# Optimization experiments

Measured on AMD Instinct MI355X. Metric: run time of the kernel, lower is better.

Reference implementation:

```python
import jax, jax.numpy as jnp
import numpy as np

B, OBS, NH, LAT = 8192, 256, 2048, 128

def setup_inputs() -> dict:
    key = jax.random.key(0)
    k1, k2, k3, k4, k5, k6 = jax.random.split(key, 6)
    s1 = 1.0 / np.sqrt(OBS + NH)
    s2 = 1.0 / np.sqrt(NH)
    return {
        "x": jax.random.normal(k1, (B, OBS), dtype=jnp.float32),
        "h": jax.random.normal(k2, (B, NH), dtype=jnp.float32),
        "W_i2h": jax.random.normal(k3, (NH, OBS + NH), dtype=jnp.float32) * s1,
        "b_i2h": jax.random.normal(k4, (NH,), dtype=jnp.float32) * s1,
        "W_h2o": jax.random.normal(k5, (2 * LAT, NH), dtype=jnp.float32) * s2,
        "b_h2o": jax.random.normal(k6, (2 * LAT,), dtype=jnp.float32) * s2,
    }

def reference(x, h, W_i2h, b_i2h, W_h2o, b_h2o):
    # combined = cat((x, h), dim=1)  -> [B, OBS+NH]
    combined = jnp.concatenate([x, h], axis=1)
    # h_new = tanh(i2h(combined));  Linear is y = x @ W.T + b
    h_new = jnp.tanh(combined @ W_i2h.T + b_i2h)
    out = h_new @ W_h2o.T + b_h2o  # [B, 2*LAT]
    return (out, h_new)
```

## Files before the change

### kernel.cpp

```cpp
#include <hip/hip_runtime.h>
#include <hip/hip_bf16.h>
#include <cstdint>

using bf16 = __hip_bfloat16;
typedef __attribute__((ext_vector_type(8))) short short8;
typedef __attribute__((ext_vector_type(4))) float floatx4;

static constexpr int BATCH = 8192;
static constexpr int K1    = 2304;
static constexpr int N1    = 2048;
static constexpr int K2    = 2048;
static constexpr int N2    = 256;

__device__ __forceinline__ void gload_lds16(const void* g, void* l) {
  __builtin_amdgcn_global_load_lds(
      (const __attribute__((address_space(1))) void*)g,
      (__attribute__((address_space(3))) void*)l, 16, 0, 0);
}

__device__ __forceinline__ float fast_tanh(float x) {
  float e = __builtin_amdgcn_exp2f(x * 2.8853900817779268f);
  return 1.0f - 2.0f * __builtin_amdgcn_rcpf(e + 1.0f);
}

__global__ __launch_bounds__(256) void cvt_f32_to_bf16(
    const float* __restrict__ s, bf16* __restrict__ d, int n8) {
  int i = blockIdx.x * 256 + threadIdx.x;
  if (i >= n8) return;
  const float4* sp = (const float4*)s + (size_t)i * 2;
  float4 a = sp[0], b = sp[1];
  union { short8 v; bf16 e[8]; } u;
  u.e[0] = __float2bfloat16(a.x); u.e[1] = __float2bfloat16(a.y);
  u.e[2] = __float2bfloat16(a.z); u.e[3] = __float2bfloat16(a.w);
  u.e[4] = __float2bfloat16(b.x); u.e[5] = __float2bfloat16(b.y);
  u.e[6] = __float2bfloat16(b.z); u.e[7] = __float2bfloat16(b.w);
  *(short8*)(d + (size_t)i * 8) = u.v;
}

__global__ __launch_bounds__(256) void build_combined(
    const float* __restrict__ x, const float* __restrict__ h,
    bf16* __restrict__ comb) {
  int i = blockIdx.x * 256 + threadIdx.x;
  int row  = i / 288;
  int slot = i - row * 288;
  const float* src = (slot < 32) ? (x + (size_t)row * 256 + slot * 8)
                                 : (h + (size_t)row * 2048 + (slot - 32) * 8);
  float4 a = ((const float4*)src)[0];
  float4 b = ((const float4*)src)[1];
  union { short8 v; bf16 e[8]; } u;
  u.e[0] = __float2bfloat16(a.x); u.e[1] = __float2bfloat16(a.y);
  u.e[2] = __float2bfloat16(a.z); u.e[3] = __float2bfloat16(a.w);
  u.e[4] = __float2bfloat16(b.x); u.e[5] = __float2bfloat16(b.y);
  u.e[6] = __float2bfloat16(b.z); u.e[7] = __float2bfloat16(b.w);
  *(short8*)(comb + (size_t)row * 2304 + slot * 8) = u.v;
}

__global__ __launch_bounds__(256) void bias_init(
    const float* __restrict__ bias, float* __restrict__ out) {
  int i = blockIdx.x * 256 + threadIdx.x;
  float4 b = ((const float4*)bias)[i & 63];
  ((float4*)out)[i] = b;
}

__global__ __launch_bounds__(256) void gemm1_tanh(
    const bf16* __restrict__ A, const bf16* __restrict__ W,
    const float* __restrict__ bias,
    float* __restrict__ hf32, bf16* __restrict__ hb16) {
  __shared__ bf16 As[128 * 64];
  __shared__ bf16 Bs[128 * 64];
  const int t    = threadIdx.x;
  const int lane = t & 63;
  const int wave = t >> 6;
  const int wm   = (wave & 1) * 64;
  const int wn   = (wave >> 1) * 64;
  const int quad = lane >> 4;
  const int r15  = lane & 15;
  const int srow = t >> 3;
  const int sc   = t & 7;

  const size_t Abase = (size_t)blockIdx.x * 128 * K1;
  const size_t Bbase = (size_t)blockIdx.y * 128 * K1;

  floatx4 acc[4][4];
  const floatx4 z = {0.f, 0.f, 0.f, 0.f};
#pragma unroll
  for (int i = 0; i < 4; i++)
#pragma unroll
    for (int j = 0; j < 4; j++) acc[i][j] = z;

  for (int kt = 0; kt < K1 / 64; ++kt) {
    const int k0 = kt * 64;
    __syncthreads();
#pragma unroll
    for (int it = 0; it < 4; ++it) {
      int row = it * 32 + srow;
      int gc  = k0 + ((sc ^ (row & 7)) << 3);
      gload_lds16(A + Abase + (size_t)row * K1 + gc,
                  (char*)As + it * 4096 + t * 16);
    }
#pragma unroll
    for (int it = 0; it < 4; ++it) {
      int row = it * 32 + srow;
      int gc  = k0 + ((sc ^ (row & 7)) << 3);
      gload_lds16(W + Bbase + (size_t)row * K1 + gc,
                  (char*)Bs + it * 4096 + t * 16);
    }
    __syncthreads();
#pragma unroll
    for (int ks = 0; ks < 2; ++ks) {
      short8 af[4], bfr[4];
      const int kq = ks * 4 + quad;
#pragma unroll
      for (int mt = 0; mt < 4; ++mt) {
        int row = wm + mt * 16 + r15;
        af[mt] = *(const short8*)((const char*)As + row * 128 +
                                  ((kq ^ (row & 7)) << 4));
      }
#pragma unroll
      for (int nt = 0; nt < 4; ++nt) {
        int row = wn + nt * 16 + r15;
        bfr[nt] = *(const short8*)((const char*)Bs + row * 128 +
                                   ((kq ^ (row & 7)) << 4));
      }
#pragma unroll
      for (int mt = 0; mt < 4; ++mt)
#pragma unroll
        for (int nt = 0; nt < 4; ++nt)
          acc[mt][nt] = __builtin_amdgcn_mfma_f32_16x16x32_bf16(
              af[mt], bfr[nt], acc[mt][nt], 0, 0, 0);
    }
  }

  const int gcol0 = blockIdx.y * 128 + wn;
  float bv[4];
#pragma unroll
  for (int nt = 0; nt < 4; ++nt) bv[nt] = bias[gcol0 + nt * 16 + r15];
  const size_t grow0 = (size_t)blockIdx.x * 128 + wm;
#pragma unroll
  for (int mt = 0; mt < 4; ++mt) {
#pragma unroll
    for (int i = 0; i < 4; ++i) {
      size_t gr = grow0 + mt * 16 + quad * 4 + i;
      size_t rb = gr * (size_t)N1;
#pragma unroll
      for (int nt = 0; nt < 4; ++nt) {
        int gc = gcol0 + nt * 16 + r15;
        float v = fast_tanh(acc[mt][nt][i] + bv[nt]);
        hf32[rb + gc] = v;
        hb16[rb + gc] = __float2bfloat16(v);
      }
    }
  }
}

__global__ __launch_bounds__(256) void gemm2_splitk(
    const bf16* __restrict__ A, const bf16* __restrict__ W,
    float* __restrict__ out) {
  __shared__ bf16 As[128 * 64];
  __shared__ bf16 Bs[64 * 64];
  const int t    = threadIdx.x;
  const int lane = t & 63;
  const int wave = t >> 6;
  const int wm   = (wave & 1) * 64;
  const int wn   = (wave >> 1) * 32;
  const int quad = lane >> 4;
  const int r15  = lane & 15;
  const int srow = t >> 3;
  const int sc   = t & 7;

  const size_t Abase = (size_t)blockIdx.x * 128 * K2;
  const size_t Bbase = (size_t)blockIdx.y * 64 * K2;
  const int ks0 = blockIdx.z * (K2 / 4);

  floatx4 acc[4][2];
  const floatx4 z = {0.f, 0.f, 0.f, 0.f};
#pragma unroll
  for (int i = 0; i < 4; i++) { acc[i][0] = z; acc[i][1] = z; }

  for (int kt = 0; kt < 8; ++kt) {
    const int k0 = ks0 + kt * 64;
    __syncthreads();
#pragma unroll
    for (int it = 0; it < 4; ++it) {
      int row = it * 32 + srow;
      int gc  = k0 + ((sc ^ (row & 7)) << 3);
      gload_lds16(A + Abase + (size_t)row * K2 + gc,
                  (char*)As + it * 4096 + t * 16);
    }
#pragma unroll
    for (int it = 0; it < 2; ++it) {
      int row = it * 32 + srow;
      int gc  = k0 + ((sc ^ (row & 7)) << 3);
      gload_lds16(W + Bbase + (size_t)row * K2 + gc,
                  (char*)Bs + it * 4096 + t * 16);
    }
    __syncthreads();
#pragma unroll
    for (int ks = 0; ks < 2; ++ks) {
      short8 af[4], bfr[2];
      const int kq = ks * 4 + quad;
#pragma unroll
      for (int mt = 0; mt < 4; ++mt) {
        int row = wm + mt * 16 + r15;
        af[mt] = *(const short8*)((const char*)As + row * 128 +
                                  ((kq ^ (row & 7)) << 4));
      }
#pragma unroll
      for (int nt = 0; nt < 2; ++nt) {
        int row = wn + nt * 16 + r15;
        bfr[nt] = *(const short8*)((const char*)Bs + row * 128 +
                                   ((kq ^ (row & 7)) << 4));
      }
#pragma unroll
      for (int mt = 0; mt < 4; ++mt)
#pragma unroll
        for (int nt = 0; nt < 2; ++nt)
          acc[mt][nt] = __builtin_amdgcn_mfma_f32_16x16x32_bf16(
              af[mt], bfr[nt], acc[mt][nt], 0, 0, 0);
    }
  }

  const int gcol0 = blockIdx.y * 64 + wn;
  const size_t grow0 = (size_t)blockIdx.x * 128 + wm;
#pragma unroll
  for (int mt = 0; mt < 4; ++mt) {
#pragma unroll
    for (int i = 0; i < 4; ++i) {
      size_t gr = grow0 + mt * 16 + quad * 4 + i;
      size_t rb = gr * (size_t)N2;
#pragma unroll
      for (int nt = 0; nt < 2; ++nt) {
        int gc = gcol0 + nt * 16 + r15;
        unsafeAtomicAdd(&out[rb + gc], acc[mt][nt][i]);
      }
    }
  }
}

extern "C" void kernel_launch(void* const* d_in, const int* in_sizes, int n_in,
                              void* d_out, int out_size, void* d_ws,
                              size_t ws_size, hipStream_t stream) {
  const float* x     = (const float*)d_in[0];
  const float* h     = (const float*)d_in[1];
  const float* W_i2h = (const float*)d_in[2];
  const float* b_i2h = (const float*)d_in[3];
  const float* W_h2o = (const float*)d_in[4];
  const float* b_h2o = (const float*)d_in[5];

  float* out       = (float*)d_out;
  float* hnew_f32  = out + (size_t)BATCH * N2;

  bf16* comb   = (bf16*)d_ws;
  bf16* Wi2h_b = comb + (size_t)BATCH * K1;
  bf16* Wh2o_b = Wi2h_b + (size_t)N1 * K1;
  bf16* hnew_b = Wh2o_b + (size_t)N2 * K2;

  bias_init<<<(BATCH * N2 / 4) / 256, 256, 0, stream>>>(b_h2o, out);

  build_combined<<<(BATCH * (K1 / 8)) / 256, 256, 0, stream>>>(x, h, comb);
  cvt_f32_to_bf16<<<((N1 * K1 / 8) + 255) / 256, 256, 0, stream>>>(
      W_i2h, Wi2h_b, N1 * K1 / 8);
  cvt_f32_to_bf16<<<((N2 * K2 / 8) + 255) / 256, 256, 0, stream>>>(
      W_h2o, Wh2o_b, N2 * K2 / 8);

  gemm1_tanh<<<dim3(BATCH / 128, N1 / 128), 256, 0, stream>>>(
      comb, Wi2h_b, b_i2h, hnew_f32, hnew_b);

  gemm2_splitk<<<dim3(BATCH / 128, N2 / 64, 4), 256, 0, stream>>>(
      hnew_b, Wh2o_b, out);
}
```

Measured before the change: 297.3 us.

## Merge conversion kernels into one prep launch and retile second GEMM

The three fp32-to-bf16 conversion kernels become one launch that picks its segment from the thread index, removing two kernel launches and their gaps. The second GEMM is retiled so each block covers 32 rows and all 256 output columns, with split-K reduced from 4 to 2. Each block now reads its A rows once instead of once per column tile, and there are half as many atomic adds per output. The cost is loading the full 256-row W tile into LDS every k-step, and the new 256x2 grid has less parallelism per block.

```diff
diff --git a/kernel.cpp b/kernel.cpp
--- a/kernel.cpp
+++ b/kernel.cpp
@@ -23,28 +23,7 @@
   return 1.0f - 2.0f * __builtin_amdgcn_rcpf(e + 1.0f);
 }
 
-__global__ __launch_bounds__(256) void cvt_f32_to_bf16(
-    const float* __restrict__ s, bf16* __restrict__ d, int n8) {
-  int i = blockIdx.x * 256 + threadIdx.x;
-  if (i >= n8) return;
-  const float4* sp = (const float4*)s + (size_t)i * 2;
-  float4 a = sp[0], b = sp[1];
-  union { short8 v; bf16 e[8]; } u;
-  u.e[0] = __float2bfloat16(a.x); u.e[1] = __float2bfloat16(a.y);
-  u.e[2] = __float2bfloat16(a.z); u.e[3] = __float2bfloat16(a.w);
-  u.e[4] = __float2bfloat16(b.x); u.e[5] = __float2bfloat16(b.y);
-  u.e[6] = __float2bfloat16(b.z); u.e[7] = __float2bfloat16(b.w);
-  *(short8*)(d + (size_t)i * 8) = u.v;
-}
-
-__global__ __launch_bounds__(256) void build_combined(
-    const float* __restrict__ x, const float* __restrict__ h,
-    bf16* __restrict__ comb) {
-  int i = blockIdx.x * 256 + threadIdx.x;
-  int row  = i / 288;
-  int slot = i - row * 288;
-  const float* src = (slot < 32) ? (x + (size_t)row * 256 + slot * 8)
-                                 : (h + (size_t)row * 2048 + (slot - 32) * 8);
+__device__ __forceinline__ short8 cvt8(const float* src) {
   float4 a = ((const float4*)src)[0];
   float4 b = ((const float4*)src)[1];
   union { short8 v; bf16 e[8]; } u;
@@ -52,7 +31,30 @@
   u.e[2] = __float2bfloat16(a.z); u.e[3] = __float2bfloat16(a.w);
   u.e[4] = __float2bfloat16(b.x); u.e[5] = __float2bfloat16(b.y);
   u.e[6] = __float2bfloat16(b.z); u.e[7] = __float2bfloat16(b.w);
-  *(short8*)(comb + (size_t)row * 2304 + slot * 8) = u.v;
+  return u.v;
+}
+
+static constexpr int SEG0 = BATCH * (K1 / 8);
+static constexpr int SEG1 = N1 * K1 / 8;
+static constexpr int SEG2 = N2 * K2 / 8;
+__global__ __launch_bounds__(256) void prep(
+    const float* __restrict__ x, const float* __restrict__ h,
+    const float* __restrict__ W1, const float* __restrict__ W2,
+    bf16* __restrict__ comb, bf16* __restrict__ W1b, bf16* __restrict__ W2b) {
+  int i = blockIdx.x * 256 + threadIdx.x;
+  if (i < SEG0) {
+    int row  = i / 288;
+    int slot = i - row * 288;
+    const float* src = (slot < 32) ? (x + (size_t)row * 256 + slot * 8)
+                                   : (h + (size_t)row * 2048 + (slot - 32) * 8);
+    *(short8*)(comb + (size_t)row * 2304 + slot * 8) = cvt8(src);
+  } else if (i < SEG0 + SEG1) {
+    int j = i - SEG0;
+    *(short8*)(W1b + (size_t)j * 8) = cvt8(W1 + (size_t)j * 8);
+  } else {
+    int j = i - (SEG0 + SEG1);
+    *(short8*)(W2b + (size_t)j * 8) = cvt8(W2 + (size_t)j * 8);
+  }
 }
 
 __global__ __launch_bounds__(256) void bias_init(
@@ -153,83 +155,79 @@
   }
 }
 
-__global__ __launch_bounds__(256) void gemm2_splitk(
+__global__ __launch_bounds__(256) void gemm2_out(
     const bf16* __restrict__ A, const bf16* __restrict__ W,
     float* __restrict__ out) {
-  __shared__ bf16 As[128 * 64];
-  __shared__ bf16 Bs[64 * 64];
+  __shared__ bf16 As[32 * 64];
+  __shared__ bf16 Bs[256 * 64];
   const int t    = threadIdx.x;
   const int lane = t & 63;
   const int wave = t >> 6;
-  const int wm   = (wave & 1) * 64;
-  const int wn   = (wave >> 1) * 32;
   const int quad = lane >> 4;
   const int r15  = lane & 15;
   const int srow = t >> 3;
   const int sc   = t & 7;
 
-  const size_t Abase = (size_t)blockIdx.x * 128 * K2;
-  const size_t Bbase = (size_t)blockIdx.y * 64 * K2;
-  const int ks0 = blockIdx.z * (K2 / 4);
-
-  floatx4 acc[4][2];
+  const int mrow0 = blockIdx.x * 32;
+  const int kbase = blockIdx.y * (K2 / 2);
+
+  floatx4 acc[2][4];
   const floatx4 z = {0.f, 0.f, 0.f, 0.f};
 #pragma unroll
-  for (int i = 0; i < 4; i++) { acc[i][0] = z; acc[i][1] = z; }
-
-  for (int kt = 0; kt < 8; ++kt) {
-    const int k0 = ks0 + kt * 64;
-    __syncthreads();
-#pragma unroll
-    for (int it = 0; it < 4; ++it) {
+  for (int i = 0; i < 2; i++)
+#pragma unroll
+    for (int j = 0; j < 4; j++) acc[i][j] = z;
+
+  for (int kt = 0; kt < 16; ++kt) {
+    const int k0 = kbase + kt * 64;
+    __syncthreads();
+    {
+      int row = srow;
+      int gc  = k0 + ((sc ^ (row & 7)) << 3);
+      gload_lds16(A + (size_t)(mrow0 + row) * K2 + gc, (char*)As + t * 16);
+    }
+#pragma unroll
+    for (int it = 0; it < 8; ++it) {
       int row = it * 32 + srow;
       int gc  = k0 + ((sc ^ (row & 7)) << 3);
-      gload_lds16(A + Abase + (size_t)row * K2 + gc,
-                  (char*)As + it * 4096 + t * 16);
-    }
-#pragma unroll
-    for (int it = 0; it < 2; ++it) {
-      int row = it * 32 + srow;
-      int gc  = k0 + ((sc ^ (row & 7)) << 3);
-      gload_lds16(W + Bbase + (size_t)row * K2 + gc,
+      gload_lds16(W + (size_t)row * K2 + gc,
                   (char*)Bs + it * 4096 + t * 16);
     }
     __syncthreads();
 #pragma unroll
     for (int ks = 0; ks < 2; ++ks) {
-      short8 af[4], bfr[2];
+      short8 af[2], bfr[4];
       const int kq = ks * 4 + quad;
 #pragma unroll
-      for (int mt = 0; mt < 4; ++mt) {
-        int row = wm + mt * 16 + r15;
+      for (int mt = 0; mt < 2; ++mt) {
+        int row = mt * 16 + r15;
         af[mt] = *(const short8*)((const char*)As + row * 128 +
                                   ((kq ^ (row & 7)) << 4));
       }
 #pragma unroll
-      for (int nt = 0; nt < 2; ++nt) {
-        int row = wn + nt * 16 + r15;
+      for (int nt = 0; nt < 4; ++nt) {
+        int row = wave * 64 + nt * 16 + r15;
         bfr[nt] = *(const short8*)((const char*)Bs + row * 128 +
                                    ((kq ^ (row & 7)) << 4));
       }
 #pragma unroll
-      for (int mt = 0; mt < 4; ++mt)
-#pragma unroll
-        for (int nt = 0; nt < 2; ++nt)
+      for (int mt = 0; mt < 2; ++mt)
+#pragma unroll
+        for (int nt = 0; nt < 4; ++nt)
           acc[mt][nt] = __builtin_amdgcn_mfma_f32_16x16x32_bf16(
               af[mt], bfr[nt], acc[mt][nt], 0, 0, 0);
     }
   }
 
-  const int gcol0 = blockIdx.y * 64 + wn;
-  const size_t grow0 = (size_t)blockIdx.x * 128 + wm;
-#pragma unroll
-  for (int mt = 0; mt < 4; ++mt) {
+  const int gcol0 = wave * 64;
+#pragma unroll
+  for (int mt = 0; mt < 2; ++mt) {
 #pragma unroll
     for (int i = 0; i < 4; ++i) {
-      size_t gr = grow0 + mt * 16 + quad * 4 + i;
+      size_t gr = (size_t)mrow0 + mt * 16 + quad * 4 + i;
       size_t rb = gr * (size_t)N2;
 #pragma unroll
-      for (int nt = 0; nt < 2; ++nt) {
+      for (int nt = 0; nt < 4; ++nt) {
         int gc = gcol0 + nt * 16 + r15;
         unsafeAtomicAdd(&out[rb + gc], acc[mt][nt][i]);
       }
@@ -257,15 +255,11 @@
 
   bias_init<<<(BATCH * N2 / 4) / 256, 256, 0, stream>>>(b_h2o, out);
 
-  build_combined<<<(BATCH * (K1 / 8)) / 256, 256, 0, stream>>>(x, h, comb);
-  cvt_f32_to_bf16<<<((N1 * K1 / 8) + 255) / 256, 256, 0, stream>>>(
-      W_i2h, Wi2h_b, N1 * K1 / 8);
-  cvt_f32_to_bf16<<<((N2 * K2 / 8) + 255) / 256, 256, 0, stream>>>(
-      W_h2o, Wh2o_b, N2 * K2 / 8);
+  prep<<<(SEG0 + SEG1 + SEG2) / 256, 256, 0, stream>>>(
+      x, h, W_i2h, W_h2o, comb, Wi2h_b, Wh2o_b);
 
   gemm1_tanh<<<dim3(BATCH / 128, N1 / 128), 256, 0, stream>>>(
       comb, Wi2h_b, b_i2h, hnew_f32, hnew_b);
 
-  gemm2_splitk<<<dim3(BATCH / 128, N2 / 64, 4), 256, 0, stream>>>(
-      hnew_b, Wh2o_b, out);
-}
+  gemm2_out<<<dim3(BATCH / 32, 2), 256, 0, stream>>>(hnew_b, Wh2o_b, out);
+}
```

Measured after the change: 276.9 us. 6.8% less time.
